# Performance work log

Hardware: AMD Instinct MI355X
Metric: run time of the kernel (lower is better)

The kernel has to match this reference:

```python
import jax, jax.numpy as jnp
import numpy as np

N_NODES = 100000
N_EDGES = 640000
D_IN, D_HID, D_OUT = 128, 128, 128


def setup_inputs() -> dict:
    key = jax.random.key(0)
    ks = jax.random.split(key, 8)
    x = jax.random.normal(ks[0], (N_NODES, D_IN), dtype=jnp.float32)
    edge_index = jax.random.randint(ks[1], (2, N_EDGES), 0, N_NODES, dtype=jnp.int64)
    s_in = 1.0 / np.sqrt(D_IN)
    s_hid = 1.0 / np.sqrt(D_HID)
    # PyG SAGEConv: lin_l applied to mean-aggregated neighbors (has bias),
    # lin_r applied to root/self features (no bias).
    W1_l = jax.random.uniform(ks[2], (D_HID, D_IN), minval=-s_in, maxval=s_in, dtype=jnp.float32)
    W1_r = jax.random.uniform(ks[3], (D_HID, D_IN), minval=-s_in, maxval=s_in, dtype=jnp.float32)
    b1 = jax.random.uniform(ks[4], (D_HID,), minval=-s_in, maxval=s_in, dtype=jnp.float32)
    W2_l = jax.random.uniform(ks[5], (D_OUT, D_HID), minval=-s_hid, maxval=s_hid, dtype=jnp.float32)
    W2_r = jax.random.uniform(ks[6], (D_OUT, D_HID), minval=-s_hid, maxval=s_hid, dtype=jnp.float32)
    b2 = jax.random.uniform(ks[7], (D_OUT,), minval=-s_hid, maxval=s_hid, dtype=jnp.float32)
    return {"x": x, "edge_index": edge_index,
            "W1_l": W1_l, "W1_r": W1_r, "b1": b1,
            "W2_l": W2_l, "W2_r": W2_r, "b2": b2}


def _sage_conv(h, src, dst, W_l, W_r, b, num_nodes):
    # gather messages from source nodes, mean-aggregate onto destinations
    msg = h[src]                                               # [E, d]
    agg = jax.ops.segment_sum(msg, dst, num_segments=num_nodes)  # [N, d]
    cnt = jax.ops.segment_sum(jnp.ones((src.shape[0],), h.dtype), dst,
                              num_segments=num_nodes)            # [N]
    mean = agg / jnp.maximum(cnt, 1.0)[:, None]
    return mean @ W_l.T + b + h @ W_r.T


def reference(x, edge_index, W1_l, W1_r, b1, W2_l, W2_r, b2):
    src, dst = edge_index[0], edge_index[1]
    n = x.shape[0]
    h = jax.nn.relu(_sage_conv(x, src, dst, W1_l, W1_r, b1, n))
    out = _sage_conv(h, src, dst, W2_l, W2_r, b2, n)
    return out
```

## Files before the change

kernel.cpp:

```cpp
#include <hip/hip_runtime.h>
#include <cstddef>


typedef __attribute__((ext_vector_type(8))) short bf16x8;
typedef __attribute__((ext_vector_type(4))) float f32x4;
typedef __attribute__((ext_vector_type(4))) unsigned int u32x4;

__device__ __forceinline__ unsigned pack_hi(float x, float y) {
    return (__float_as_uint(x) >> 16) | (__float_as_uint(y) & 0xFFFF0000u);
}
__device__ __forceinline__ float hi_part(float x) {
    return __uint_as_float(__float_as_uint(x) & 0xFFFF0000u);
}

__global__ void zero_kernel(float4* __restrict__ p, long n4) {
    long i = (long)blockIdx.x * blockDim.x + threadIdx.x;
    long stride = (long)gridDim.x * blockDim.x;
    float4 z = {0.f, 0.f, 0.f, 0.f};
    for (; i < n4; i += stride) p[i] = z;
}

__global__ void prep_wfrag(const float* __restrict__ Wl, const float* __restrict__ Wr,
                           unsigned short* __restrict__ hi, unsigned short* __restrict__ lo) {
    int t = blockIdx.x * 256 + threadIdx.x;
    int lane = t & 63;
    int nf = (t >> 6) & 7;
    int col = nf * 16 + (lane & 15);
    int kb = (t >> 9) * 32 + (lane >> 4) * 8;
    unsigned hv[4], lv[4];
#pragma unroll
    for (int jj = 0; jj < 4; jj++) {
        int k0 = kb + 2 * jj, k1 = k0 + 1;
        float a0 = (k0 < 128) ? Wl[col * 128 + k0] : Wr[col * 128 + (k0 - 128)];
        float a1 = (k1 < 128) ? Wl[col * 128 + k1] : Wr[col * 128 + (k1 - 128)];
        hv[jj] = pack_hi(a0, a1);
        lv[jj] = pack_hi(a0 - hi_part(a0), a1 - hi_part(a1));
    }
    u32x4 h = {hv[0], hv[1], hv[2], hv[3]};
    u32x4 l = {lv[0], lv[1], lv[2], lv[3]};
    reinterpret_cast<u32x4*>(hi)[t] = h;
    reinterpret_cast<u32x4*>(lo)[t] = l;
}


__global__ void hist_kernel(const int* __restrict__ ei, int* __restrict__ cnt, int E) {
    int e = blockIdx.x * 256 + threadIdx.x;
    if (e < E) atomicAdd(&cnt[ei[E + e]], 1);
}

__global__ void scan1(const int* __restrict__ cnt, int* __restrict__ blockSums, int M) {
    __shared__ int red[256];
    const int t = threadIdx.x;
    const int base = blockIdx.x * 1024 + t * 4;
    int s = 0;
#pragma unroll
    for (int i = 0; i < 4; i++) { int idx = base + i; if (idx < M) s += cnt[idx]; }
    red[t] = s; __syncthreads();
    for (int off = 128; off > 0; off >>= 1) {
        if (t < off) red[t] += red[t + off];
        __syncthreads();
    }
    if (t == 0) blockSums[blockIdx.x] = red[0];
}

__global__ void scan2(int* __restrict__ bs, int NB) {
    __shared__ int tmp[256];
    const int t = threadIdx.x;
    int v = (t < NB) ? bs[t] : 0;
    tmp[t] = v; __syncthreads();
    for (int off = 1; off < 256; off <<= 1) {
        int add = (t >= off) ? tmp[t - off] : 0;
        __syncthreads();
        tmp[t] += add;
        __syncthreads();
    }
    if (t < NB) bs[t] = tmp[t] - v;
}

__global__ void scan3(const int* __restrict__ cnt, const int* __restrict__ blockSums,
                      int* __restrict__ rowStart, int* __restrict__ cursor, int M) {
    __shared__ int tsum[256];
    const int t = threadIdx.x;
    const int base = blockIdx.x * 1024 + t * 4;
    int v[4];
#pragma unroll
    for (int i = 0; i < 4; i++) v[i] = (base + i < M) ? cnt[base + i] : 0;
    const int s = v[0] + v[1] + v[2] + v[3];
    tsum[t] = s; __syncthreads();
    for (int off = 1; off < 256; off <<= 1) {
        int add = (t >= off) ? tsum[t - off] : 0;
        __syncthreads();
        tsum[t] += add;
        __syncthreads();
    }
    int rs = blockSums[blockIdx.x] + (tsum[t] - s);
#pragma unroll
    for (int i = 0; i < 4; i++) {
        int idx = base + i;
        if (idx < M) {
            rowStart[idx] = rs;
            cursor[idx]   = rs;
            rs += v[i];
            if (idx == M - 1) rowStart[M] = rs;
        }
    }
}

__global__ void scatter_kernel(const int* __restrict__ ei, int* __restrict__ cursor,
                               int* __restrict__ csr, int E) {
    int e = blockIdx.x * 256 + threadIdx.x;
    if (e < E) {
        int d = ei[E + e];
        int pos = atomicAdd(&cursor[d], 1);
        csr[pos] = ei[e];
    }
}

__global__ void csr_aggregate(const float* __restrict__ feat,
                              const int* __restrict__ rowStart,
                              const int* __restrict__ csr,
                              float* __restrict__ mean, int M) {
    int n = blockIdx.x * (blockDim.x >> 6) + (threadIdx.x >> 6);
    if (n >= M) return;
    const int lane = threadIdx.x & 63;
    const int beg = rowStart[n], end = rowStart[n + 1];
    const int deg = end - beg;

    int myidx = (beg + lane < end) ? csr[beg + lane] : 0;
    float2 acc = {0.f, 0.f};
    const int K = deg < 64 ? deg : 64;
    for (int p = 0; p < K; p++) {
        int s = __shfl(myidx, p);
        const float2 v = *reinterpret_cast<const float2*>(&feat[(size_t)s * 128 + lane * 2]);
        acc.x += v.x; acc.y += v.y;
    }
    for (int q = beg + 64; q < end; q++) {
        int s = csr[q];
        const float2 v = *reinterpret_cast<const float2*>(&feat[(size_t)s * 128 + lane * 2]);
        acc.x += v.x; acc.y += v.y;
    }
    const float inv = 1.0f / fmaxf((float)deg, 1.0f);
    acc.x *= inv; acc.y *= inv;
    *reinterpret_cast<float2*>(&mean[(size_t)n * 128 + lane * 2]) = acc;
}

template <bool RELU>
__global__ __launch_bounds__(256, 2)
void sage_gemm_mfma(const float* __restrict__ mean, const float* __restrict__ selfF,
                    const unsigned short* __restrict__ wHi,
                    const unsigned short* __restrict__ wLo,
                    const float* __restrict__ bias,
                    float* __restrict__ out, int M) {
    __shared__ unsigned short aHi[4096];
    __shared__ unsigned short aLo[4096];

    const int tid  = threadIdx.x;
    const int lane = tid & 63;
    const int wid  = tid >> 6;
    const int wm   = wid >> 1;
    const int wn   = wid & 1;
    const int row0 = blockIdx.x * 128;

    const int sr = tid >> 1;
    const int sh = tid & 1;
    const int arow = row0 + sr;
    const bool av = arow < M;
    const float* mrow = mean  + (size_t)arow * 128 + sh * 16;
    const float* srow = selfF + (size_t)arow * 128 + sh * 16;
    const int wslot = (sr >> 4) * 64 + (sr & 15) + (2 * sh) * 16;

    f32x4 acc[4][4];
#pragma unroll
    for (int i = 0; i < 4; i++)
#pragma unroll
        for (int j = 0; j < 4; j++) acc[i][j] = {0.f, 0.f, 0.f, 0.f};

    float4 r[4], rn[4];
#pragma unroll
    for (int i = 0; i < 4; i++) { r[i] = {0.f,0.f,0.f,0.f}; rn[i] = {0.f,0.f,0.f,0.f}; }
    if (av) {
#pragma unroll
        for (int i = 0; i < 4; i++) r[i] = reinterpret_cast<const float4*>(mrow)[i];
    }

    const bf16x8* WH = reinterpret_cast<const bf16x8*>(wHi);
    const bf16x8* WL = reinterpret_cast<const bf16x8*>(wLo);
    const bf16x8* AH = reinterpret_cast<const bf16x8*>(aHi);
    const bf16x8* AL = reinterpret_cast<const bf16x8*>(aLo);

    for (int ks = 0; ks < 8; ks++) {
        u32x4 h0 = {pack_hi(r[0].x, r[0].y), pack_hi(r[0].z, r[0].w),
                    pack_hi(r[1].x, r[1].y), pack_hi(r[1].z, r[1].w)};
        u32x4 h1 = {pack_hi(r[2].x, r[2].y), pack_hi(r[2].z, r[2].w),
                    pack_hi(r[3].x, r[3].y), pack_hi(r[3].z, r[3].w)};
        u32x4 l0 = {pack_hi(r[0].x - hi_part(r[0].x), r[0].y - hi_part(r[0].y)),
                    pack_hi(r[0].z - hi_part(r[0].z), r[0].w - hi_part(r[0].w)),
                    pack_hi(r[1].x - hi_part(r[1].x), r[1].y - hi_part(r[1].y)),
                    pack_hi(r[1].z - hi_part(r[1].z), r[1].w - hi_part(r[1].w))};
        u32x4 l1 = {pack_hi(r[2].x - hi_part(r[2].x), r[2].y - hi_part(r[2].y)),
                    pack_hi(r[2].z - hi_part(r[2].z), r[2].w - hi_part(r[2].w)),
                    pack_hi(r[3].x - hi_part(r[3].x), r[3].y - hi_part(r[3].y)),
                    pack_hi(r[3].z - hi_part(r[3].z), r[3].w - hi_part(r[3].w))};

        if (ks) __syncthreads();
        reinterpret_cast<u32x4*>(aHi)[wslot]      = h0;
        reinterpret_cast<u32x4*>(aHi)[wslot + 16] = h1;
        reinterpret_cast<u32x4*>(aLo)[wslot]      = l0;
        reinterpret_cast<u32x4*>(aLo)[wslot + 16] = l1;

        if (ks < 7) {
            const int k0n = (ks + 1) * 32;
            const float* src = (k0n < 128) ? (mrow + k0n) : (srow + (k0n - 128));
            if (av) {
#pragma unroll
                for (int i = 0; i < 4; i++) rn[i] = reinterpret_cast<const float4*>(src)[i];
            }
        }
        __syncthreads();

        bf16x8 bh[4], bl[4], ah[4], al[4];
#pragma unroll
        for (int nfl = 0; nfl < 4; nfl++) {
            const int bidx = (ks * 8 + wn * 4 + nfl) * 64 + lane;
            bh[nfl] = WH[bidx];
            bl[nfl] = WL[bidx];
        }
#pragma unroll
        for (int mfl = 0; mfl < 4; mfl++) {
            const int aidx = (wm * 4 + mfl) * 64 + lane;
            ah[mfl] = AH[aidx];
            al[mfl] = AL[aidx];
        }
#pragma unroll
        for (int mfl = 0; mfl < 4; mfl++)
#pragma unroll
            for (int nfl = 0; nfl < 4; nfl++) {
                acc[mfl][nfl] = __builtin_amdgcn_mfma_f32_16x16x32_bf16(
                    ah[mfl], bh[nfl], acc[mfl][nfl], 0, 0, 0);
                acc[mfl][nfl] = __builtin_amdgcn_mfma_f32_16x16x32_bf16(
                    al[mfl], bh[nfl], acc[mfl][nfl], 0, 0, 0);
                acc[mfl][nfl] = __builtin_amdgcn_mfma_f32_16x16x32_bf16(
                    ah[mfl], bl[nfl], acc[mfl][nfl], 0, 0, 0);
            }
#pragma unroll
        for (int i = 0; i < 4; i++) r[i] = rn[i];
    }

    const int colb = wn * 64 + (lane & 15);
    const int rowb = row0 + wm * 64 + ((lane >> 4) << 2);
#pragma unroll
    for (int nfl = 0; nfl < 4; nfl++) {
        const float bv = bias[colb + nfl * 16];
#pragma unroll
        for (int mfl = 0; mfl < 4; mfl++) {
#pragma unroll
            for (int q = 0; q < 4; q++) {
                const int row = rowb + mfl * 16 + q;
                if (row < M) {
                    float v = acc[mfl][nfl][q] + bv;
                    if (RELU) v = fmaxf(v, 0.0f);
                    out[(size_t)row * 128 + colb + nfl * 16] = v;
                }
            }
        }
    }
}

extern "C" void kernel_launch(void* const* d_in, const int* in_sizes, int n_in,
                              void* d_out, int out_size, void* d_ws, size_t ws_size,
                              hipStream_t stream) {
    const float* x   = (const float*)d_in[0];
    const int*   ei  = (const int*)d_in[1];
    const float* W1l = (const float*)d_in[2];
    const float* W1r = (const float*)d_in[3];
    const float* b1  = (const float*)d_in[4];
    const float* W2l = (const float*)d_in[5];
    const float* W2r = (const float*)d_in[6];
    const float* b2  = (const float*)d_in[7];
    float* out = (float*)d_out;

    const int M = in_sizes[0] / 128;
    const int E = in_sizes[1] / 2;
    const int NB = (M + 1023) / 1024;
    const size_t featBytes = (size_t)M * 128 * sizeof(float);
    const size_t al = 512;
    auto rup = [&](size_t b) { return (b + al - 1) & ~(al - 1); };

    char* ws = (char*)d_ws;
    size_t off = 0;
    int* cntHist  = (int*)(ws + off); off += rup((size_t)M * 4);
    int* rowStart = (int*)(ws + off); off += rup((size_t)(M + 1) * 4);
    int* cursor   = (int*)(ws + off); off += rup((size_t)M * 4);
    int* blockSum = (int*)(ws + off); off += rup(256 * 4);
    int* csr      = (int*)(ws + off); off += rup((size_t)E * 4);
    float* mean   = (float*)(ws + off); off += featBytes;
    float* h      = (float*)(ws + off); off += featBytes;
    unsigned short* w1hi = (unsigned short*)(ws + off); off += 256 * 128 * 2;
    unsigned short* w1lo = (unsigned short*)(ws + off); off += 256 * 128 * 2;
    unsigned short* w2hi = (unsigned short*)(ws + off); off += 256 * 128 * 2;
    unsigned short* w2lo = (unsigned short*)(ws + off); off += 256 * 128 * 2;

    prep_wfrag<<<16, 256, 0, stream>>>(W1l, W1r, w1hi, w1lo);
    prep_wfrag<<<16, 256, 0, stream>>>(W2l, W2r, w2hi, w2lo);

    zero_kernel<<<128, 256, 0, stream>>>((float4*)cntHist, (long)(rup((size_t)M * 4) / 16));
    hist_kernel<<<(E + 255) / 256, 256, 0, stream>>>(ei, cntHist, E);
    scan1<<<NB, 256, 0, stream>>>(cntHist, blockSum, M);
    scan2<<<1, 256, 0, stream>>>(blockSum, NB);
    scan3<<<NB, 256, 0, stream>>>(cntHist, blockSum, rowStart, cursor, M);
    scatter_kernel<<<(E + 255) / 256, 256, 0, stream>>>(ei, cursor, csr, E);

    csr_aggregate<<<(M + 3) / 4, 256, 0, stream>>>(x, rowStart, csr, mean, M);
    sage_gemm_mfma<true><<<(M + 127) / 128, 256, 0, stream>>>(mean, x, w1hi, w1lo, b1, h, M);

    csr_aggregate<<<(M + 3) / 4, 256, 0, stream>>>(h, rowStart, csr, mean, M);
    sage_gemm_mfma<false><<<(M + 127) / 128, 256, 0, stream>>>(mean, h, w2hi, w2lo, b2, out, M);
}
```

Before: 407.7 us.

## Store intermediates as split bf16 hi/lo planes and aggregate with half-wave float4 gathers

The mean and hidden features are now written as two bf16 planes (hi and residual lo) instead of fp32, so the GEMM loads pre-split operands and skips the per-element split arithmetic. The CSR aggregation processes two neighbors per wave, each half-wave gathering a full row with float4 loads, then combines the halves with a cross-half shuffle. Storage size is unchanged since two 16-bit planes equal one fp32 plane. The hi+lo representation drops some low-order mantissa bits, and the scattered 2-byte stores in the GEMM epilogue may be less efficient than the former fp32 stores.

```diff
diff --git a/kernel.cpp b/kernel.cpp
--- a/kernel.cpp
+++ b/kernel.cpp
@@ -11,6 +11,9 @@
 }
 __device__ __forceinline__ float hi_part(float x) {
     return __uint_as_float(__float_as_uint(x) & 0xFFFF0000u);
+}
+__device__ __forceinline__ float bf2f(unsigned short u) {
+    return __uint_as_float(((unsigned)u) << 16);
 }
 
 __global__ void zero_kernel(float4* __restrict__ p, long n4) {
@@ -116,41 +119,100 @@
     }
 }
 
+template <bool SPLIT_IN>
 __global__ void csr_aggregate(const float* __restrict__ feat,
+                              const unsigned short* __restrict__ fHi,
+                              const unsigned short* __restrict__ fLo,
                               const int* __restrict__ rowStart,
                               const int* __restrict__ csr,
-                              float* __restrict__ mean, int M) {
+                              unsigned short* __restrict__ mHi,
+                              unsigned short* __restrict__ mLo, int M) {
     int n = blockIdx.x * (blockDim.x >> 6) + (threadIdx.x >> 6);
     if (n >= M) return;
     const int lane = threadIdx.x & 63;
+    const int half = lane >> 5;
+    const int cl   = lane & 31;
     const int beg = rowStart[n], end = rowStart[n + 1];
     const int deg = end - beg;
 
     int myidx = (beg + lane < end) ? csr[beg + lane] : 0;
-    float2 acc = {0.f, 0.f};
-    const int K = deg < 64 ? deg : 64;
-    for (int p = 0; p < K; p++) {
-        int s = __shfl(myidx, p);
-        const float2 v = *reinterpret_cast<const float2*>(&feat[(size_t)s * 128 + lane * 2]);
-        acc.x += v.x; acc.y += v.y;
-    }
-    for (int q = beg + 64; q < end; q++) {
-        int s = csr[q];
-        const float2 v = *reinterpret_cast<const float2*>(&feat[(size_t)s * 128 + lane * 2]);
-        acc.x += v.x; acc.y += v.y;
-    }
+
+    auto loadRow = [&](int s) -> float4 {
+        if constexpr (!SPLIT_IN) {
+            return *reinterpret_cast<const float4*>(feat + (size_t)s * 128 + cl * 4);
+        } else {
+            ushort4 hh = *reinterpret_cast<const ushort4*>(fHi + (size_t)s * 128 + cl * 4);
+            ushort4 ll = *reinterpret_cast<const ushort4*>(fLo + (size_t)s * 128 + cl * 4);
+            float4 v;
+            v.x = bf2f(hh.x) + bf2f(ll.x);
+            v.y = bf2f(hh.y) + bf2f(ll.y);
+            v.z = bf2f(hh.z) + bf2f(ll.z);
+            v.w = bf2f(hh.w) + bf2f(ll.w);
+            return v;
+        }
+    };
+
+    float4 a0 = {0.f, 0.f, 0.f, 0.f}, a1 = {0.f, 0.f, 0.f, 0.f};
+    const int K  = deg < 64 ? deg : 64;
+    const int NP = (K + 1) >> 1;
+    int p = 0;
+    for (; p + 1 < NP; p += 2) {
+        const int nb0 = 2 * p + half;
+        const int nb1 = nb0 + 2;
+        const int s0 = __shfl(myidx, nb0);
+        const int s1 = __shfl(myidx, nb1);
+        if (nb0 < K) { float4 v = loadRow(s0); a0.x += v.x; a0.y += v.y; a0.z += v.z; a0.w += v.w; }
+        if (nb1 < K) { float4 v = loadRow(s1); a1.x += v.x; a1.y += v.y; a1.z += v.z; a1.w += v.w; }
+    }
+    if (p < NP) {
+        const int nb = 2 * p + half;
+        const int s = __shfl(myidx, nb);
+        if (nb < K) { float4 v = loadRow(s); a0.x += v.x; a0.y += v.y; a0.z += v.z; a0.w += v.w; }
+    }
+    for (int q = beg + 64 + half; q < end; q += 2) {
+        float4 v = loadRow(csr[q]);
+        a0.x += v.x; a0.y += v.y; a0.z += v.z; a0.w += v.w;
+    }
+    a0.x += a1.x; a0.y += a1.y; a0.z += a1.z; a0.w += a1.w;
+
+    a0.x += __shfl_xor(a0.x, 32);
+    a0.y += __shfl_xor(a0.y, 32);
+    a0.z += __shfl_xor(a0.z, 32);
+    a0.w += __shfl_xor(a0.w, 32);
+
     const float inv = 1.0f / fmaxf((float)deg, 1.0f);
-    acc.x *= inv; acc.y *= inv;
-    *reinterpret_cast<float2*>(&mean[(size_t)n * 128 + lane * 2]) = acc;
-}
-
-template <bool RELU>
+    float m[4] = {a0.x * inv, a0.y * inv, a0.z * inv, a0.w * inv};
+
+    ushort4 st;
+    if (half == 0) {
+        st.x = __float_as_uint(m[0]) >> 16;
+        st.y = __float_as_uint(m[1]) >> 16;
+        st.z = __float_as_uint(m[2]) >> 16;
+        st.w = __float_as_uint(m[3]) >> 16;
+        *reinterpret_cast<ushort4*>(mHi + (size_t)n * 128 + cl * 4) = st;
+    } else {
+        st.x = __float_as_uint(m[0] - hi_part(m[0])) >> 16;
+        st.y = __float_as_uint(m[1] - hi_part(m[1])) >> 16;
+        st.z = __float_as_uint(m[2] - hi_part(m[2])) >> 16;
+        st.w = __float_as_uint(m[3] - hi_part(m[3])) >> 16;
+        *reinterpret_cast<ushort4*>(mLo + (size_t)n * 128 + cl * 4) = st;
+    }
+}
+
+template <bool RELU, bool SELF_F32, bool SPLIT_OUT>
 __global__ __launch_bounds__(256, 2)
-void sage_gemm_mfma(const float* __restrict__ mean, const float* __restrict__ selfF,
+void sage_gemm_mfma(const unsigned short* __restrict__ mHi,
+                    const unsigned short* __restrict__ mLo,
+                    const float* __restrict__ selfF,
+                    const unsigned short* __restrict__ sHi,
+                    const unsigned short* __restrict__ sLo,
                     const unsigned short* __restrict__ wHi,
                     const unsigned short* __restrict__ wLo,
                     const float* __restrict__ bias,
-                    float* __restrict__ out, int M) {
+                    float* __restrict__ outF,
+                    unsigned short* __restrict__ outHi,
+                    unsigned short* __restrict__ outLo,
+                    int M) {
     __shared__ unsigned short aHi[4096];
     __shared__ unsigned short aLo[4096];
 
@@ -165,8 +227,7 @@
     const int sh = tid & 1;
     const int arow = row0 + sr;
     const bool av = arow < M;
-    const float* mrow = mean  + (size_t)arow * 128 + sh * 16;
-    const float* srow = selfF + (size_t)arow * 128 + sh * 16;
+    const size_t rb = (size_t)arow * 128 + sh * 16;
     const int wslot = (sr >> 4) * 64 + (sr & 15) + (2 * sh) * 16;
 
     f32x4 acc[4][4];
@@ -175,47 +236,59 @@
 #pragma unroll
         for (int j = 0; j < 4; j++) acc[i][j] = {0.f, 0.f, 0.f, 0.f};
 
-    float4 r[4], rn[4];
-#pragma unroll
-    for (int i = 0; i < 4; i++) { r[i] = {0.f,0.f,0.f,0.f}; rn[i] = {0.f,0.f,0.f,0.f}; }
-    if (av) {
-#pragma unroll
-        for (int i = 0; i < 4; i++) r[i] = reinterpret_cast<const float4*>(mrow)[i];
-    }
+    u32x4 h0, h1, l0, l1, nh0, nh1, nl0, nl1;
+
+    auto loadA = [&](int ks, u32x4& H0, u32x4& H1, u32x4& L0, u32x4& L1) {
+        if (!av) { H0 = H1 = L0 = L1 = (u32x4){0u, 0u, 0u, 0u}; return; }
+        const int k0 = ks * 32;
+        if (k0 < 128) {
+            const unsigned short* ph = mHi + rb + k0;
+            const unsigned short* pl = mLo + rb + k0;
+            H0 = *reinterpret_cast<const u32x4*>(ph);
+            H1 = *reinterpret_cast<const u32x4*>(ph + 8);
+            L0 = *reinterpret_cast<const u32x4*>(pl);
+            L1 = *reinterpret_cast<const u32x4*>(pl + 8);
+        } else if constexpr (!SELF_F32) {
+            const unsigned short* ph = sHi + rb + (k0 - 128);
+            const unsigned short* pl = sLo + rb + (k0 - 128);
+            H0 = *reinterpret_cast<const u32x4*>(ph);
+            H1 = *reinterpret_cast<const u32x4*>(ph + 8);
+            L0 = *reinterpret_cast<const u32x4*>(pl);
+            L1 = *reinterpret_cast<const u32x4*>(pl + 8);
+        } else {
+            const float* ps = selfF + rb + (k0 - 128);
+            float4 r0 = reinterpret_cast<const float4*>(ps)[0];
+            float4 r1 = reinterpret_cast<const float4*>(ps)[1];
+            float4 r2 = reinterpret_cast<const float4*>(ps)[2];
+            float4 r3 = reinterpret_cast<const float4*>(ps)[3];
+            H0 = (u32x4){pack_hi(r0.x, r0.y), pack_hi(r0.z, r0.w),
+                         pack_hi(r1.x, r1.y), pack_hi(r1.z, r1.w)};
+            H1 = (u32x4){pack_hi(r2.x, r2.y), pack_hi(r2.z, r2.w),
+                         pack_hi(r3.x, r3.y), pack_hi(r3.z, r3.w)};
+            L0 = (u32x4){pack_hi(r0.x - hi_part(r0.x), r0.y - hi_part(r0.y)),
+                         pack_hi(r0.z - hi_part(r0.z), r0.w - hi_part(r0.w)),
+                         pack_hi(r1.x - hi_part(r1.x), r1.y - hi_part(r1.y)),
+                         pack_hi(r1.z - hi_part(r1.z), r1.w - hi_part(r1.w))};
+            L1 = (u32x4){pack_hi(r2.x - hi_part(r2.x), r2.y - hi_part(r2.y)),
+                         pack_hi(r2.z - hi_part(r2.z), r2.w - hi_part(r2.w)),
+                         pack_hi(r3.x - hi_part(r3.x), r3.y - hi_part(r3.y)),
+                         pack_hi(r3.z - hi_part(r3.z), r3.w - hi_part(r3.w))};
+        }
+    };
 
     const bf16x8* WH = reinterpret_cast<const bf16x8*>(wHi);
     const bf16x8* WL = reinterpret_cast<const bf16x8*>(wLo);
     const bf16x8* AH = reinterpret_cast<const bf16x8*>(aHi);
     const bf16x8* AL = reinterpret_cast<const bf16x8*>(aLo);
 
+    loadA(0, h0, h1, l0, l1);
     for (int ks = 0; ks < 8; ks++) {
-        u32x4 h0 = {pack_hi(r[0].x, r[0].y), pack_hi(r[0].z, r[0].w),
-                    pack_hi(r[1].x, r[1].y), pack_hi(r[1].z, r[1].w)};
-        u32x4 h1 = {pack_hi(r[2].x, r[2].y), pack_hi(r[2].z, r[2].w),
-                    pack_hi(r[3].x, r[3].y), pack_hi(r[3].z, r[3].w)};
-        u32x4 l0 = {pack_hi(r[0].x - hi_part(r[0].x), r[0].y - hi_part(r[0].y)),
-                    pack_hi(r[0].z - hi_part(r[0].z), r[0].w - hi_part(r[0].w)),
-                    pack_hi(r[1].x - hi_part(r[1].x), r[1].y - hi_part(r[1].y)),
-                    pack_hi(r[1].z - hi_part(r[1].z), r[1].w - hi_part(r[1].w))};
-        u32x4 l1 = {pack_hi(r[2].x - hi_part(r[2].x), r[2].y - hi_part(r[2].y)),
-                    pack_hi(r[2].z - hi_part(r[2].z), r[2].w - hi_part(r[2].w)),
-                    pack_hi(r[3].x - hi_part(r[3].x), r[3].y - hi_part(r[3].y)),
-                    pack_hi(r[3].z - hi_part(r[3].z), r[3].w - hi_part(r[3].w))};
-
         if (ks) __syncthreads();
         reinterpret_cast<u32x4*>(aHi)[wslot]      = h0;
         reinterpret_cast<u32x4*>(aHi)[wslot + 16] = h1;
         reinterpret_cast<u32x4*>(aLo)[wslot]      = l0;
         reinterpret_cast<u32x4*>(aLo)[wslot + 16] = l1;
-
-        if (ks < 7) {
-            const int k0n = (ks + 1) * 32;
-            const float* src = (k0n < 128) ? (mrow + k0n) : (srow + (k0n - 128));
-            if (av) {
-#pragma unroll
-                for (int i = 0; i < 4; i++) rn[i] = reinterpret_cast<const float4*>(src)[i];
-            }
-        }
+        if (ks < 7) loadA(ks + 1, nh0, nh1, nl0, nl1);
         __syncthreads();
 
         bf16x8 bh[4], bl[4], ah[4], al[4];
@@ -242,8 +315,7 @@
                 acc[mfl][nfl] = __builtin_amdgcn_mfma_f32_16x16x32_bf16(
                     ah[mfl], bl[nfl], acc[mfl][nfl], 0, 0, 0);
             }
-#pragma unroll
-        for (int i = 0; i < 4; i++) r[i] = rn[i];
+        h0 = nh0; h1 = nh1; l0 = nl0; l1 = nl1;
     }
 
     const int colb = wn * 64 + (lane & 15);
@@ -259,7 +331,15 @@
                 if (row < M) {
                     float v = acc[mfl][nfl][q] + bv;
                     if (RELU) v = fmaxf(v, 0.0f);
-                    out[(size_t)row * 128 + colb + nfl * 16] = v;
+                    const size_t idx = (size_t)row * 128 + colb + nfl * 16;
+                    if constexpr (!SPLIT_OUT) {
+                        outF[idx] = v;
+                    } else {
+                        const unsigned u = __float_as_uint(v);
+                        outHi[idx] = (unsigned short)(u >> 16);
+                        const float fh = __uint_as_float(u & 0xFFFF0000u);
+                        outLo[idx] = (unsigned short)(__float_as_uint(v - fh) >> 16);
+                    }
                 }
             }
         }
@@ -282,7 +362,7 @@
     const int M = in_sizes[0] / 128;
     const int E = in_sizes[1] / 2;
     const int NB = (M + 1023) / 1024;
-    const size_t featBytes = (size_t)M * 128 * sizeof(float);
+    const size_t planeBytes = (size_t)M * 128 * sizeof(unsigned short);
     const size_t al = 512;
     auto rup = [&](size_t b) { return (b + al - 1) & ~(al - 1); };
 
@@ -293,8 +373,10 @@
     int* cursor   = (int*)(ws + off); off += rup((size_t)M * 4);
     int* blockSum = (int*)(ws + off); off += rup(256 * 4);
     int* csr      = (int*)(ws + off); off += rup((size_t)E * 4);
-    float* mean   = (float*)(ws + off); off += featBytes;
-    float* h      = (float*)(ws + off); off += featBytes;
+    unsigned short* meanHi = (unsigned short*)(ws + off); off += rup(planeBytes);
+    unsigned short* meanLo = (unsigned short*)(ws + off); off += rup(planeBytes);
+    unsigned short* hHi    = (unsigned short*)(ws + off); off += rup(planeBytes);
+    unsigned short* hLo    = (unsigned short*)(ws + off); off += rup(planeBytes);
     unsigned short* w1hi = (unsigned short*)(ws + off); off += 256 * 128 * 2;
     unsigned short* w1lo = (unsigned short*)(ws + off); off += 256 * 128 * 2;
     unsigned short* w2hi = (unsigned short*)(ws + off); off += 256 * 128 * 2;
@@ -310,9 +392,13 @@
     scan3<<<NB, 256, 0, stream>>>(cntHist, blockSum, rowStart, cursor, M);
     scatter_kernel<<<(E + 255) / 256, 256, 0, stream>>>(ei, cursor, csr, E);
 
-    csr_aggregate<<<(M + 3) / 4, 256, 0, stream>>>(x, rowStart, csr, mean, M);
-    sage_gemm_mfma<true><<<(M + 127) / 128, 256, 0, stream>>>(mean, x, w1hi, w1lo, b1, h, M);
-
-    csr_aggregate<<<(M + 3) / 4, 256, 0, stream>>>(h, rowStart, csr, mean, M);
-    sage_gemm_mfma<false><<<(M + 127) / 128, 256, 0, stream>>>(mean, h, w2hi, w2lo, b2, out, M);
-}
+    csr_aggregate<false><<<(M + 3) / 4, 256, 0, stream>>>(
+        x, nullptr, nullptr, rowStart, csr, meanHi, meanLo, M);
+    sage_gemm_mfma<true, true, true><<<(M + 127) / 128, 256, 0, stream>>>(
+        meanHi, meanLo, x, nullptr, nullptr, w1hi, w1lo, b1, nullptr, hHi, hLo, M);
+
+    csr_aggregate<true><<<(M + 3) / 4, 256, 0, stream>>>(
+        nullptr, hHi, hLo, rowStart, csr, meanHi, meanLo, M);
+    sage_gemm_mfma<false, false, false><<<(M + 127) / 128, 256, 0, stream>>>(
+        meanHi, meanLo, nullptr, hHi, hLo, w2hi, w2lo, b2, out, nullptr, nullptr, M);
+}
```

Result: no change. 402.9 us (-1.2%).
